# Kernel optimization log

Hardware: AMD Instinct MI355X
Metric: run time of the kernel (lower is better)

## Reference

```python
import jax, jax.numpy as jnp
import numpy as np

EPS = 1e-6  # added only where the 2-way softmax prob is exactly zero (matches torch code)

def setup_inputs() -> dict:
    key = jax.random.key(0)
    k1, k2 = jax.random.split(key)
    B, C = 65536, 1000  # nClass = 1000, input has C+1 logits
    input = jax.random.normal(k1, (B, C + 1), dtype=jnp.float32)
    target = jax.random.randint(k2, (B,), 0, C)  # unused in the math, shape-only
    return {"input": input, "target": target}

def reference(input, target):
    B = input.shape[0]
    logits = input[:, :-1]            # [B, C] class logits
    extra = input[:, -1:]             # [B, 1] shared extra logit
    prob = jax.nn.softmax(logits, axis=1)               # [B, C]
    # 2-way softmax([input[:,i], input[:,-1]])[-1] == sigmoid(extra - logits[:,i])
    pc = jax.nn.sigmoid(extra - logits)                  # [B, C] prob of extra class
    pc_adj = jnp.where(pc == 0, pc + EPS, pc)            # torch adds 1e-6 only where exactly 0
    # sum over classes of per-class batch means == total sum / B
    loss = -(prob * jnp.log(pc_adj)).sum() / B
    return loss
```

## Files before the change

### kernel.cpp

```cpp
#include <hip/hip_runtime.h>
#include <math.h>

#define ROWS 65536
#define COLS 1000
#define STRIDE 1001
#define K1_BLOCKS 2048
#define WAVES_PER_BLOCK 4
#define EPSV 1e-6f

__global__ __launch_bounds__(256) void row_loss_kernel(
    const float* __restrict__ in, float* __restrict__ partial) {
    const int lane  = threadIdx.x & 63;
    const int wave  = threadIdx.x >> 6;
    const int gwave = blockIdx.x * WAVES_PER_BLOCK + wave;
    const int nwaves = gridDim.x * WAVES_PER_BLOCK;

    float wsum = 0.0f;
    for (int row = gwave; row < ROWS; row += nwaves) {
        const float* rp = in + (size_t)row * STRIDE;

        float l[16];
        #pragma unroll
        for (int k = 0; k < 16; ++k) {
            int c = lane + 64 * k;
            l[k] = (c < COLS) ? rp[c] : -INFINITY;
        }
        float extra = rp[COLS];

        float m = l[0];
        #pragma unroll
        for (int k = 1; k < 16; ++k) m = fmaxf(m, l[k]);
        #pragma unroll
        for (int off = 32; off > 0; off >>= 1) m = fmaxf(m, __shfl_xor(m, off));

        float e[16];
        float se = 0.0f;
        #pragma unroll
        for (int k = 0; k < 16; ++k) {
            int c = lane + 64 * k;
            float v = (c < COLS) ? __expf(l[k] - m) : 0.0f;
            e[k] = v;
            se += v;
        }
        #pragma unroll
        for (int off = 32; off > 0; off >>= 1) se += __shfl_xor(se, off);
        float rdenom = 1.0f / se;

        float t = 0.0f;
        #pragma unroll
        for (int k = 0; k < 16; ++k) {
            int c = lane + 64 * k;
            if (c < COLS) {
                float p = e[k] * rdenom;
                float x = extra - l[k];
                float s = __builtin_amdgcn_rcpf(1.0f + __expf(-x));
                if (s == 0.0f) s = EPSV;
                t += p * __logf(s);
            }
        }
        #pragma unroll
        for (int off = 32; off > 0; off >>= 1) t += __shfl_xor(t, off);
        wsum += t;
    }

    __shared__ float sdata[WAVES_PER_BLOCK];
    if (lane == 0) sdata[wave] = wsum;
    __syncthreads();
    if (threadIdx.x == 0) {
        float b = 0.0f;
        #pragma unroll
        for (int w = 0; w < WAVES_PER_BLOCK; ++w) b += sdata[w];
        partial[blockIdx.x] = b;
    }
}

__global__ __launch_bounds__(256) void final_reduce(
    const float* __restrict__ partial, float* __restrict__ out) {
    float s = 0.0f;
    for (int i = threadIdx.x; i < K1_BLOCKS; i += 256) s += partial[i];
    #pragma unroll
    for (int off = 32; off > 0; off >>= 1) s += __shfl_xor(s, off);
    __shared__ float sdata[4];
    const int lane = threadIdx.x & 63, wave = threadIdx.x >> 6;
    if (lane == 0) sdata[wave] = s;
    __syncthreads();
    if (threadIdx.x == 0) {
        float tot = sdata[0] + sdata[1] + sdata[2] + sdata[3];
        out[0] = -tot / (float)ROWS;
    }
}

extern "C" void kernel_launch(void* const* d_in, const int* in_sizes, int n_in,
                              void* d_out, int out_size, void* d_ws, size_t ws_size,
                              hipStream_t stream) {
    const float* in = (const float*)d_in[0];
    float* partial = (float*)d_ws;
    row_loss_kernel<<<K1_BLOCKS, 256, 0, stream>>>(in, partial);
    final_reduce<<<1, 256, 0, stream>>>(partial, (float*)d_out);
}
```

Before: 358.6 us.

## Single-pass row loss with float4 loads and fused softmax-weighted log-sigmoid

```diff
diff --git a/kernel.cpp b/kernel.cpp
--- a/kernel.cpp
+++ b/kernel.cpp
@@ -4,63 +4,60 @@
 #define ROWS 65536
 #define COLS 1000
 #define STRIDE 1001
-#define K1_BLOCKS 2048
+#define TOTAL_ELEMS ((size_t)ROWS * STRIDE)
+#define K1_BLOCKS 4096
 #define WAVES_PER_BLOCK 4
-#define EPSV 1e-6f
+#define ROWS_PER_WAVE 4
 
 __global__ __launch_bounds__(256) void row_loss_kernel(
     const float* __restrict__ in, float* __restrict__ partial) {
     const int lane  = threadIdx.x & 63;
     const int wave  = threadIdx.x >> 6;
     const int gwave = blockIdx.x * WAVES_PER_BLOCK + wave;
-    const int nwaves = gridDim.x * WAVES_PER_BLOCK;
+    const int nwaves = K1_BLOCKS * WAVES_PER_BLOCK;
 
     float wsum = 0.0f;
-    for (int row = gwave; row < ROWS; row += nwaves) {
-        const float* rp = in + (size_t)row * STRIDE;
+    #pragma unroll 1
+    for (int i = 0; i < ROWS_PER_WAVE; ++i) {
+        const int row = gwave + i * nwaves;
+        const size_t rowstart = (size_t)row * STRIDE;
+        const size_t a0 = rowstart & ~(size_t)3;
+        const int p = (int)(rowstart - a0);
 
-        float l[16];
+        float4 v[4];
         #pragma unroll
-        for (int k = 0; k < 16; ++k) {
-            int c = lane + 64 * k;
-            l[k] = (c < COLS) ? rp[c] : -INFINITY;
+        for (int j = 0; j < 4; ++j) {
+            size_t g = a0 + (size_t)(256 * j + 4 * lane);
+            if (g > TOTAL_ELEMS - 4) g = TOTAL_ELEMS - 4;
+            v[j] = *(const float4*)(in + g);
         }
-        float extra = rp[COLS];
 
-        float m = l[0];
+        float ev = (p == 0) ? v[3].x : (p == 1) ? v[3].y
+                 : (p == 2) ? v[3].z : v[3].w;
+        float extra = __shfl(ev, 58);
+
+        float S1 = 0.0f, S2 = 0.0f;
         #pragma unroll
-        for (int k = 1; k < 16; ++k) m = fmaxf(m, l[k]);
-        #pragma unroll
-        for (int off = 32; off > 0; off >>= 1) m = fmaxf(m, __shfl_xor(m, off));
-
-        float e[16];
-        float se = 0.0f;
-        #pragma unroll
-        for (int k = 0; k < 16; ++k) {
-            int c = lane + 64 * k;
-            float v = (c < COLS) ? __expf(l[k] - m) : 0.0f;
-            e[k] = v;
-            se += v;
-        }
-        #pragma unroll
-        for (int off = 32; off > 0; off >>= 1) se += __shfl_xor(se, off);
-        float rdenom = 1.0f / se;
-
-        float t = 0.0f;
-        #pragma unroll
-        for (int k = 0; k < 16; ++k) {
-            int c = lane + 64 * k;
-            if (c < COLS) {
-                float p = e[k] * rdenom;
-                float x = extra - l[k];
-                float s = __builtin_amdgcn_rcpf(1.0f + __expf(-x));
-                if (s == 0.0f) s = EPSV;
-                t += p * __logf(s);
+        for (int j = 0; j < 4; ++j) {
+            const float* vv = (const float*)&v[j];
+            #pragma unroll
+            for (int t = 0; t < 4; ++t) {
+                int g = 256 * j + 4 * lane + t;
+                bool valid = (g >= p) && (g < p + COLS);
+                float l  = vv[t];
+                float e  = valid ? __expf(l) : 0.0f;
+                float ls = -__logf(1.0f + __expf(l - extra));
+                S1 += e;
+                S2 += e * ls;
             }
         }
+
         #pragma unroll
-        for (int off = 32; off > 0; off >>= 1) t += __shfl_xor(t, off);
-        wsum += t;
+        for (int off = 32; off > 0; off >>= 1) {
+            S1 += __shfl_xor(S1, off);
+            S2 += __shfl_xor(S2, off);
+        }
+        wsum += S2 / S1;
     }
 
     __shared__ float sdata[WAVES_PER_BLOCK];
```

Measured after the change: 359.8 us. About the same (+0.3%).
